# Kernel optimization log

Measured on AMD Instinct MI355X. Metric: run time of the kernel, lower is better.

Reference implementation:

```python
import jax, jax.numpy as jnp
import numpy as np

H_DIM = 1024
HEAD_DIM = 128
N_HEADS = 8
HD = HEAD_DIM * N_HEADS  # 1024


def setup_inputs() -> dict:
    key = jax.random.key(0)
    ks = jax.random.split(key, 32)
    B, S = 16, 1024
    inp = {
        "f_in": jax.random.normal(ks[0], (B, S, H_DIM), jnp.float32),
        "i_in": jax.random.normal(ks[1], (B, S, H_DIM), jnp.float32),
        "z_in": jax.random.normal(ks[2], (B, S, H_DIM), jnp.float32),
        "o_in": jax.random.normal(ks[3], (B, S, H_DIM), jnp.float32),
        "c0": jax.random.normal(ks[4], (B, N_HEADS, HEAD_DIM), jnp.float32),
        "h0": jax.random.normal(ks[5], (B, N_HEADS, HEAD_DIM), jnp.float32),
    }
    # Parameters (torch Linear stored here as [in, out]; init std=0.02, zero bias)
    names_x = ["Fx", "Ix", "Zx", "Ox"]
    names_h = ["Fh", "Ih", "Zh", "Oh"]
    for j, n in enumerate(names_x):
        inp[f"W_{n}"] = 0.02 * jax.random.normal(ks[6 + j], (H_DIM, HD), jnp.float32)
        inp[f"b_{n}"] = jnp.zeros((HD,), jnp.float32)
    for j, n in enumerate(names_h):
        inp[f"W_{n}"] = 0.02 * jax.random.normal(ks[10 + j], (HD, HD), jnp.float32)
        inp[f"b_{n}"] = jnp.zeros((HD,), jnp.float32)
    inp["W_post"] = 0.02 * jax.random.normal(ks[14], (HD, H_DIM), jnp.float32)
    inp["b_post"] = jnp.zeros((H_DIM,), jnp.float32)
    return inp


def reference(f_in, i_in, z_in, o_in, c0, h0,
              W_Fx, b_Fx, W_Ix, b_Ix, W_Zx, b_Zx, W_Ox, b_Ox,
              W_Fh, b_Fh, W_Ih, b_Ih, W_Zh, b_Zh, W_Oh, b_Oh,
              W_post, b_post):
    B, S, _ = f_in.shape
    # Precompute input-to-gate projections for all timesteps: (B,S,HD)
    fx = f_in @ W_Fx + b_Fx
    ix = i_in @ W_Ix + b_Ix
    zx = z_in @ W_Zx + b_Zx
    ox = o_in @ W_Ox + b_Ox
    # Flatten head state: gating is elementwise, heads are contiguous in HD
    c = c0.reshape(B, HD)
    h = h0.reshape(B, HD)
    # Time-major for scan: (S,B,HD)
    xs = (fx.transpose(1, 0, 2), ix.transpose(1, 0, 2),
          zx.transpose(1, 0, 2), ox.transpose(1, 0, 2))

    def step(carry, x):
        c, h = carry
        fx_t, ix_t, zx_t, ox_t = x
        f = jax.nn.sigmoid(fx_t + h @ W_Fh + b_Fh)
        i = jax.nn.sigmoid(ix_t + h @ W_Ih + b_Ih)
        z = jnp.tanh(zx_t + h @ W_Zh + b_Zh)
        o = jax.nn.sigmoid(ox_t + h @ W_Oh + b_Oh)
        c = f * c + i * z
        h = o * jnp.tanh(c)
        return (c, h), h

    (c, h), ys = jax.lax.scan(step, (c, h), xs)
    y = ys.transpose(1, 0, 2)  # (B,S,HD)
    y = y @ W_post + b_post    # n_heads > 1 -> post-head projection
    state = (c.reshape(B, N_HEADS, HEAD_DIM), h.reshape(B, N_HEADS, HEAD_DIM))
    return (y, state)
```

## Files before the change

### kernel.cpp

```cpp
#include <hip/hip_runtime.h>
#include <stdint.h>
#include <stddef.h>

typedef __attribute__((ext_vector_type(8))) short short8;
typedef __attribute__((ext_vector_type(4))) short short4_t;
typedef __attribute__((ext_vector_type(8))) unsigned short ushort8_t;
typedef __attribute__((ext_vector_type(4))) unsigned short ushort4_t;
typedef __attribute__((ext_vector_type(4))) float f32x4;
typedef __attribute__((ext_vector_type(4))) unsigned uint4_t;

#define XG_BYTES  (134217728ull)
#define HS_BYTES  (33587200ull)
#define PAD_OFF   (XG_BYTES + HS_BYTES)
#define WT_OFF    (PAD_OFF + 32768ull)

#define SENT 0x7FC07FC0u

__device__ __forceinline__ unsigned short f2b(float f){
  unsigned u = __builtin_bit_cast(unsigned, f);
  u += 0x7fffu + ((u >> 16) & 1u);
  return (unsigned short)(u >> 16);
}
__device__ __forceinline__ float b2f(unsigned short b){
  unsigned u = ((unsigned)b) << 16;
  return __builtin_bit_cast(float, u);
}
__device__ __forceinline__ float sigm(float x){ return 1.0f / (1.0f + __expf(-x)); }
__device__ __forceinline__ float tanh_(float x){ return 2.0f / (1.0f + __expf(-2.0f*x)) - 1.0f; }

__device__ __forceinline__ void ld_h8_plain(const unsigned short* p, short8* a){
  asm volatile(
    "global_load_dwordx4 %0, %8, off\n\t"
    "global_load_dwordx4 %1, %8, off offset:64\n\t"
    "global_load_dwordx4 %2, %8, off offset:128\n\t"
    "global_load_dwordx4 %3, %8, off offset:192\n\t"
    "global_load_dwordx4 %4, %8, off offset:256\n\t"
    "global_load_dwordx4 %5, %8, off offset:320\n\t"
    "global_load_dwordx4 %6, %8, off offset:384\n\t"
    "global_load_dwordx4 %7, %8, off offset:448\n\t"
    "s_waitcnt vmcnt(0)"
    : "=&v"(a[0]), "=&v"(a[1]), "=&v"(a[2]), "=&v"(a[3]),
      "=&v"(a[4]), "=&v"(a[5]), "=&v"(a[6]), "=&v"(a[7])
    : "v"(p) : "memory");
}
__device__ __forceinline__ void st_u32_mall(unsigned* p, unsigned v){
  asm volatile("global_store_dword %0, %1, off sc0 sc1"
               :: "v"(p), "v"(v) : "memory");
}

__global__ __launch_bounds__(256) void k_prep(
    const float* __restrict__ w0, const float* __restrict__ w1,
    const float* __restrict__ w2, const float* __restrict__ w3,
    const float* __restrict__ w4, const float* __restrict__ w5,
    const float* __restrict__ w6, const float* __restrict__ w7,
    const float* __restrict__ w8, unsigned short* __restrict__ wt)
{
  const int z = blockIdx.z;
  const float* W = (z==0)?w0:(z==1)?w1:(z==2)?w2:(z==3)?w3:(z==4)?w4:
                   (z==5)?w5:(z==6)?w6:(z==7)?w7:w8;
  unsigned short* out = wt + (size_t)z*1024*1024;
  __shared__ float tile[64][65];
  const int k0 = blockIdx.x*64, n0 = blockIdx.y*64;
  const int tid = threadIdx.x;
  {
    const int kk = tid >> 2, nn0 = (tid & 3) * 16;
    const float* src = W + (size_t)(k0+kk)*1024 + n0 + nn0;
    #pragma unroll
    for (int j=0;j<16;j+=4){
      f32x4 v = *(const f32x4*)(src + j);
      tile[kk][nn0+j+0]=v[0]; tile[kk][nn0+j+1]=v[1];
      tile[kk][nn0+j+2]=v[2]; tile[kk][nn0+j+3]=v[3];
    }
  }
  __syncthreads();
  {
    const int nn = tid >> 2, kk0 = (tid & 3) * 16;
    ushort8_t a, b;
    #pragma unroll
    for (int j=0;j<8;++j){ a[j]=f2b(tile[kk0+j][nn]); b[j]=f2b(tile[kk0+8+j][nn]); }
    unsigned short* dst = out + (size_t)(n0+nn)*1024 + k0 + kk0;
    *(ushort8_t*)dst = a;
    *(ushort8_t*)(dst+8) = b;
  }
}

__global__ void k_init(const float* __restrict__ h0, unsigned short* __restrict__ hs){
  const int i = blockIdx.x*256 + threadIdx.x;
  unsigned v = (unsigned)f2b(h0[i]);
  asm volatile("global_store_short %0, %1, off sc0 sc1"
               :: "v"(hs + i), "v"(v) : "memory");
}

__global__ void k_fill(unsigned* __restrict__ hsw){
  const size_t i = (size_t)blockIdx.x*256 + threadIdx.x;
  uint4_t v = (uint4_t){SENT, SENT, SENT, SENT};
  asm volatile("global_store_dwordx4 %0, %1, off sc0 sc1"
               :: "v"(hsw + 8192 + i*4), "v"(v) : "memory");
}

__global__ __launch_bounds__(256,2) void k_xproj(
    const float* __restrict__ xF, const float* __restrict__ xI,
    const float* __restrict__ xZ, const float* __restrict__ xO,
    const float* __restrict__ bF, const float* __restrict__ bI,
    const float* __restrict__ bZ, const float* __restrict__ bO,
    const unsigned short* __restrict__ Wt,
    unsigned short* __restrict__ xg)
{
  const int g  = blockIdx.z;
  const int tm = blockIdx.x, tn = blockIdx.y;
  const float* X  = (g==0)?xF:(g==1)?xI:(g==2)?xZ:xO;
  const float* Bp = (g==0)?bF:(g==1)?bI:(g==2)?bZ:bO;
  const unsigned short* Wg = Wt + (size_t)g*1024*1024;

  __shared__ unsigned short Asm[128*32];
  __shared__ unsigned short Bsm[128*32];

  const int tid  = threadIdx.x;
  const int lane = tid & 63, wv = tid >> 6;
  const int l15  = lane & 15, lg = lane >> 4;
  const int wy   = wv >> 1,  wx = wv & 1;

  const int rr = tid >> 1, kq = tid & 1;
  const int ar = tm*128 + rr;
  const int ab = ar & 15, as_ = ar >> 4;
  const float* aptr = X + ((size_t)ab*1024 + as_)*1024 + kq*16;
  const unsigned short* bp_ = Wg + (size_t)(tn*128 + rr)*1024 + kq*16;
  const int s0 = kq*2;
  unsigned short* aw0 = &Asm[rr*32 + (((s0  ) ^ (rr&3))<<3)];
  unsigned short* aw1 = &Asm[rr*32 + (((s0+1) ^ (rr&3))<<3)];
  unsigned short* bw0 = &Bsm[rr*32 + (((s0  ) ^ (rr&3))<<3)];
  unsigned short* bw1 = &Bsm[rr*32 + (((s0+1) ^ (rr&3))<<3)];

  f32x4 acc[4][4];
  #pragma unroll
  for (int m=0;m<4;++m)
    #pragma unroll
    for (int q=0;q<4;++q) acc[m][q] = (f32x4){0.f,0.f,0.f,0.f};

  for (int k0=0; k0<1024; k0+=32){
    const float* ap = aptr + k0;
    f32x4 v0 = *(const f32x4*)(ap + 0);
    f32x4 v1 = *(const f32x4*)(ap + 4);
    f32x4 v2 = *(const f32x4*)(ap + 8);
    f32x4 v3 = *(const f32x4*)(ap + 12);
    ushort8_t pa, pb;
    #pragma unroll
    for (int j=0;j<4;++j){ pa[j]=f2b(v0[j]); pa[4+j]=f2b(v1[j]); pb[j]=f2b(v2[j]); pb[4+j]=f2b(v3[j]); }
    *(ushort8_t*)aw0 = pa;
    *(ushort8_t*)aw1 = pb;
    ushort8_t q0 = *(const ushort8_t*)(bp_ + k0);
    ushort8_t q1 = *(const ushort8_t*)(bp_ + k0 + 8);
    *(ushort8_t*)bw0 = q0;
    *(ushort8_t*)bw1 = q1;
    __syncthreads();

    short8 af[4], bf_[4];
    #pragma unroll
    for (int m=0;m<4;++m){
      int row = wy*64 + m*16 + l15;
      af[m] = *(const short8*)&Asm[row*32 + ((lg ^ (row&3))<<3)];
    }
    #pragma unroll
    for (int q=0;q<4;++q){
      int row = wx*64 + q*16 + l15;
      bf_[q] = *(const short8*)&Bsm[row*32 + ((lg ^ (row&3))<<3)];
    }
    #pragma unroll
    for (int m=0;m<4;++m)
      #pragma unroll
      for (int q=0;q<4;++q)
        acc[m][q] = __builtin_amdgcn_mfma_f32_16x16x32_bf16(af[m], bf_[q], acc[m][q], 0,0,0);
    __syncthreads();
  }

  #pragma unroll
  for (int m=0;m<4;++m){
    const int t = tm*8 + wy*4 + m;
    #pragma unroll
    for (int q=0;q<4;++q){
      const int n = tn*128 + wx*64 + q*16 + l15;
      const float bias = Bp[n];
      f32x4 v = acc[m][q];
      ushort4_t pk;
      #pragma unroll
      for (int r=0;r<4;++r) pk[r] = f2b(v[r] + bias);
      *(ushort4_t*)(xg + (size_t)((t*4+g)*1024 + n)*16 + lg*4) = pk;
    }
  }
}

__global__ __launch_bounds__(256,1) void k_recur(
    const unsigned short* __restrict__ WtR,
    const float* __restrict__ bfh, const float* __restrict__ bih,
    const float* __restrict__ bzh, const float* __restrict__ boh,
    const float* __restrict__ c0,
    const unsigned short* __restrict__ xg,
    unsigned short* __restrict__ hs,
    float* __restrict__ oc, float* __restrict__ oh)
{
  const int wg   = blockIdx.x;
  const int tid  = threadIdx.x;
  const int wv   = tid >> 6, lane = tid & 63;
  const int l15  = lane & 15, lg = lane >> 4;
  const int n    = wg*16 + l15;

  short8 wf[4][8];
  #pragma unroll
  for (int g=0; g<4; ++g){
    const unsigned short* wp = WtR + (size_t)g*1048576 + (size_t)n*1024 + wv*256 + lg*8;
    #pragma unroll
    for (int c=0; c<8; ++c)
      wf[g][c] = *(const short8*)(wp + c*32);
  }

  float cst[4]; float bias[4];
  bias[0]=bfh[n]; bias[1]=bih[n]; bias[2]=bzh[n]; bias[3]=boh[n];
  #pragma unroll
  for (int r=0;r<4;++r) cst[r] = c0[(size_t)(lg*4+r)*1024 + n];

  __shared__ f32x4 part[2][4][4][64];

  unsigned* hsw = (unsigned*)hs;
  const int koff = l15*1024 + wv*256 + lg*8;

  float hv = 0.f;
  for (int t=0; t<1024; ++t){
    short4_t xq[4];
    #pragma unroll
    for (int g=0; g<4; ++g)
      xq[g] = *(const short4_t*)(xg + (size_t)((t*4+g)*1024 + n)*16 + lg*4);

    const unsigned short* hp = hs + (size_t)t*16384 + koff;
    short8 a[8];
    ld_h8_plain(hp, a);
    {
      bool bad[8]; bool any = false;
      #pragma unroll
      for (int c=0;c<8;++c){
        uint4_t q = __builtin_bit_cast(uint4_t, a[c]);
        bad[c] = (q[0]==SENT)||(q[1]==SENT)||(q[2]==SENT)||(q[3]==SENT);
        any = any | bad[c];
      }
      while (__any(any)){
        __builtin_amdgcn_s_sleep(1);
        #pragma unroll
        for (int c=0;c<8;++c)
          if (bad[c])
            asm volatile("global_load_dwordx4 %0, %1, off sc0 sc1"
                         : "+v"(a[c]) : "v"(hp + c*32) : "memory");
        asm volatile("s_waitcnt vmcnt(0)" ::: "memory");
        __builtin_amdgcn_sched_barrier(0);
        any = false;
        #pragma unroll
        for (int c=0;c<8;++c){
          uint4_t q = __builtin_bit_cast(uint4_t, a[c]);
          bad[c] = (q[0]==SENT)||(q[1]==SENT)||(q[2]==SENT)||(q[3]==SENT);
          any = any | bad[c];
        }
      }
    }

    f32x4 acc[4];
    #pragma unroll
    for (int g=0;g<4;++g) acc[g] = (f32x4){0.f,0.f,0.f,0.f};
    #pragma unroll
    for (int c=0;c<8;++c){
      acc[0] = __builtin_amdgcn_mfma_f32_16x16x32_bf16(a[c], wf[0][c], acc[0], 0,0,0);
      acc[1] = __builtin_amdgcn_mfma_f32_16x16x32_bf16(a[c], wf[1][c], acc[1], 0,0,0);
      acc[2] = __builtin_amdgcn_mfma_f32_16x16x32_bf16(a[c], wf[2][c], acc[2], 0,0,0);
      acc[3] = __builtin_amdgcn_mfma_f32_16x16x32_bf16(a[c], wf[3][c], acc[3], 0,0,0);
    }
    const int pb = t & 1;
    #pragma unroll
    for (int g=0;g<4;++g) part[pb][wv][g][lane] = acc[g];
    __syncthreads();

    f32x4 r_[4];
    #pragma unroll
    for (int g=0;g<4;++g){
      f32x4 s0 = part[pb][0][g][lane];
      f32x4 s1 = part[pb][1][g][lane];
      f32x4 s2 = part[pb][2][g][lane];
      f32x4 s3 = part[pb][3][g][lane];
      r_[g] = (s0 + s1) + (s2 + s3);
    }

    float hvv[4];
    {
      const int r = wv;
      float pf = r_[0][r] + b2f((unsigned short)xq[0][r]) + bias[0];
      float pi = r_[1][r] + b2f((unsigned short)xq[1][r]) + bias[1];
      float pz = r_[2][r] + b2f((unsigned short)xq[2][r]) + bias[2];
      float po = r_[3][r] + b2f((unsigned short)xq[3][r]) + bias[3];
      float fg = sigm(pf), ig = sigm(pi), zg = tanh_(pz), og = sigm(po);
      float cn = fg*cst[r] + ig*zg;
      cst[r] = cn;
      hv = og * tanh_(cn);
      hvv[r] = hv;
      unsigned m  = (unsigned)f2b(hv);
      unsigned nb = (unsigned)__shfl_xor(m, 1);
      if ((l15 & 1) == 0){
        unsigned word = m | (nb << 16);
        unsigned* pw = hsw + (size_t)(t+1)*8192 + (size_t)(lg*4+wv)*512 + (n >> 1);
        st_u32_mall(pw, word);
      }
    }
    #pragma unroll
    for (int r=0;r<4;++r){
      if (r == wv) continue;
      float pf = r_[0][r] + b2f((unsigned short)xq[0][r]) + bias[0];
      float pi = r_[1][r] + b2f((unsigned short)xq[1][r]) + bias[1];
      float pz = r_[2][r] + b2f((unsigned short)xq[2][r]) + bias[2];
      float po = r_[3][r] + b2f((unsigned short)xq[3][r]) + bias[3];
      float fg = sigm(pf), ig = sigm(pi), zg = tanh_(pz), og = sigm(po);
      float cn = fg*cst[r] + ig*zg;
      cst[r] = cn;
      hvv[r] = og * tanh_(cn);
    }
    if (t == 1023 && wv == 0){
      #pragma unroll
      for (int r=0;r<4;++r){
        oc[(size_t)(lg*4+r)*1024 + n] = cst[r];
        oh[(size_t)(lg*4+r)*1024 + n] = hvv[r];
      }
    }
  }
}

__global__ __launch_bounds__(256,2) void k_post(
    const unsigned short* __restrict__ hs,
    const unsigned short* __restrict__ Wt,
    const float* __restrict__ bpost,
    float* __restrict__ y)
{
  const int tm = blockIdx.x, tn = blockIdx.y;
  __shared__ unsigned short Asm[128*32];
  __shared__ unsigned short Bsm[128*32];

  const int tid  = threadIdx.x;
  const int lane = tid & 63, wv = tid >> 6;
  const int l15  = lane & 15, lg = lane >> 4;
  const int wy   = wv >> 1,  wx = wv & 1;

  const int rr = tid >> 1, kq = tid & 1;
  const unsigned short* aptr = hs + 16384 + (size_t)(tm*128 + rr)*1024 + kq*16;
  const unsigned short* bp_  = Wt + (size_t)4*1024*1024 + (size_t)(tn*128 + rr)*1024 + kq*16;
  const int s0 = kq*2;
  unsigned short* aw0 = &Asm[rr*32 + (((s0  ) ^ (rr&3))<<3)];
  unsigned short* aw1 = &Asm[rr*32 + (((s0+1) ^ (rr&3))<<3)];
  unsigned short* bw0 = &Bsm[rr*32 + (((s0  ) ^ (rr&3))<<3)];
  unsigned short* bw1 = &Bsm[rr*32 + (((s0+1) ^ (rr&3))<<3)];

  f32x4 acc[4][4];
  #pragma unroll
  for (int m=0;m<4;++m)
    #pragma unroll
    for (int q=0;q<4;++q) acc[m][q] = (f32x4){0.f,0.f,0.f,0.f};

  for (int k0=0; k0<1024; k0+=32){
    ushort8_t a0 = *(const ushort8_t*)(aptr + k0);
    ushort8_t a1 = *(const ushort8_t*)(aptr + k0 + 8);
    *(ushort8_t*)aw0 = a0;
    *(ushort8_t*)aw1 = a1;
    ushort8_t q0 = *(const ushort8_t*)(bp_ + k0);
    ushort8_t q1 = *(const ushort8_t*)(bp_ + k0 + 8);
    *(ushort8_t*)bw0 = q0;
    *(ushort8_t*)bw1 = q1;
    __syncthreads();

    short8 af[4], bf_[4];
    #pragma unroll
    for (int m=0;m<4;++m){
      int row = wy*64 + m*16 + l15;
      af[m] = *(const short8*)&Asm[row*32 + ((lg ^ (row&3))<<3)];
    }
    #pragma unroll
    for (int q=0;q<4;++q){
      int row = wx*64 + q*16 + l15;
      bf_[q] = *(const short8*)&Bsm[row*32 + ((lg ^ (row&3))<<3)];
    }
    #pragma unroll
    for (int m=0;m<4;++m)
      #pragma unroll
      for (int q=0;q<4;++q)
        acc[m][q] = __builtin_amdgcn_mfma_f32_16x16x32_bf16(af[m], bf_[q], acc[m][q], 0,0,0);
    __syncthreads();
  }

  #pragma unroll
  for (int m=0;m<4;++m){
    const int s = tm*8 + wy*4 + m;
    #pragma unroll
    for (int q=0;q<4;++q){
      const int n = tn*128 + wx*64 + q*16 + l15;
      const float bias = bpost[n];
      f32x4 v = acc[m][q];
      #pragma unroll
      for (int r=0;r<4;++r){
        const int b = lg*4 + r;
        y[((size_t)b << 20) + ((size_t)s << 10) + n] = v[r] + bias;
      }
    }
  }
}

extern "C" void kernel_launch(void* const* d_in, const int* in_sizes, int n_in,
                              void* d_out, int out_size, void* d_ws, size_t ws_size,
                              hipStream_t stream)
{
  const float* f_in = (const float*)d_in[0];
  const float* i_in = (const float*)d_in[1];
  const float* z_in = (const float*)d_in[2];
  const float* o_in = (const float*)d_in[3];
  const float* c0   = (const float*)d_in[4];
  const float* h0   = (const float*)d_in[5];
  const float* W_Fx = (const float*)d_in[6];  const float* b_Fx = (const float*)d_in[7];
  const float* W_Ix = (const float*)d_in[8];  const float* b_Ix = (const float*)d_in[9];
  const float* W_Zx = (const float*)d_in[10]; const float* b_Zx = (const float*)d_in[11];
  const float* W_Ox = (const float*)d_in[12]; const float* b_Ox = (const float*)d_in[13];
  const float* W_Fh = (const float*)d_in[14]; const float* b_Fh = (const float*)d_in[15];
  const float* W_Ih = (const float*)d_in[16]; const float* b_Ih = (const float*)d_in[17];
  const float* W_Zh = (const float*)d_in[18]; const float* b_Zh = (const float*)d_in[19];
  const float* W_Oh = (const float*)d_in[20]; const float* b_Oh = (const float*)d_in[21];
  const float* W_post = (const float*)d_in[22]; const float* b_post = (const float*)d_in[23];

  char* ws = (char*)d_ws;
  unsigned short* xg    = (unsigned short*)(ws);
  unsigned short* hs    = (unsigned short*)(ws + XG_BYTES);
  unsigned short* wt    = (unsigned short*)(ws + WT_OFF);

  float* y  = (float*)d_out;
  float* oc = y + 16777216;
  float* oh = oc + 16384;

  k_prep<<<dim3(16,16,9), 256, 0, stream>>>(W_Fx, W_Ix, W_Zx, W_Ox, W_post,
                                            W_Fh, W_Ih, W_Zh, W_Oh, wt);
  k_init<<<64, 256, 0, stream>>>(h0, hs);
  k_fill<<<8192, 256, 0, stream>>>((unsigned*)hs);
  k_xproj<<<dim3(128,8,4), 256, 0, stream>>>(f_in, i_in, z_in, o_in,
                                             b_Fx, b_Ix, b_Zx, b_Ox, wt, xg);
  k_recur<<<64, 256, 0, stream>>>(wt + (size_t)5*1024*1024,
                                  b_Fh, b_Ih, b_Zh, b_Oh,
                                  c0, xg, hs, oc, oh);
  k_post<<<dim3(128,8), 256, 0, stream>>>(hs, wt, b_post, y);
}
```

Measured before the change: 3.728 ms.

## Fuse xproj, recurrence and post projection into one persistent overlapped kernel

Merges the input projection, the recurrent scan and the post-head projection into a single kernel. Its first 64 blocks run the recurrence while the remaining 192 blocks compute the input GEMMs and then the post GEMM. Workspace is pre-filled with sentinel values so consumers spin on them, letting the projection and post stages overlap with the serial scan instead of running before and after it. The costs are a larger sentinel fill of the xg buffer, polling overhead, and a reliance on all 256 blocks being co-resident to avoid deadlock.

```diff
diff --git a/kernel.cpp b/kernel.cpp
--- a/kernel.cpp
+++ b/kernel.cpp
@@ -8,6 +8,7 @@
 typedef __attribute__((ext_vector_type(4))) unsigned short ushort4_t;
 typedef __attribute__((ext_vector_type(4))) float f32x4;
 typedef __attribute__((ext_vector_type(4))) unsigned uint4_t;
+typedef __attribute__((ext_vector_type(2))) unsigned uint2_t;
 
 #define XG_BYTES  (134217728ull)
 #define HS_BYTES  (33587200ull)
@@ -91,314 +92,365 @@
                :: "v"(hs + i), "v"(v) : "memory");
 }
 
-__global__ void k_fill(unsigned* __restrict__ hsw){
+__global__ void k_fill(unsigned* __restrict__ xgw, unsigned* __restrict__ hsw){
   const size_t i = (size_t)blockIdx.x*256 + threadIdx.x;
   uint4_t v = (uint4_t){SENT, SENT, SENT, SENT};
-  asm volatile("global_store_dwordx4 %0, %1, off sc0 sc1"
-               :: "v"(hsw + 8192 + i*4), "v"(v) : "memory");
-}
-
-__global__ __launch_bounds__(256,2) void k_xproj(
+  if (i < 8388608ull){
+    asm volatile("global_store_dwordx4 %0, %1, off sc0 sc1"
+                 :: "v"(xgw + i*4), "v"(v) : "memory");
+  } else {
+    asm volatile("global_store_dwordx4 %0, %1, off sc0 sc1"
+                 :: "v"(hsw + 8192 + (i - 8388608ull)*4), "v"(v) : "memory");
+  }
+}
+
+__global__ __launch_bounds__(256,1) void k_mega(
     const float* __restrict__ xF, const float* __restrict__ xI,
     const float* __restrict__ xZ, const float* __restrict__ xO,
     const float* __restrict__ bF, const float* __restrict__ bI,
     const float* __restrict__ bZ, const float* __restrict__ bO,
-    const unsigned short* __restrict__ Wt,
-    unsigned short* __restrict__ xg)
+    const unsigned short* __restrict__ wt,
+    const float* __restrict__ bfh, const float* __restrict__ bih,
+    const float* __restrict__ bzh, const float* __restrict__ boh,
+    const float* __restrict__ c0,
+    unsigned short* __restrict__ xg,
+    unsigned short* __restrict__ hs,
+    const float* __restrict__ bpost,
+    float* __restrict__ y,
+    float* __restrict__ oc, float* __restrict__ oh)
 {
-  const int g  = blockIdx.z;
-  const int tm = blockIdx.x, tn = blockIdx.y;
-  const float* X  = (g==0)?xF:(g==1)?xI:(g==2)?xZ:xO;
-  const float* Bp = (g==0)?bF:(g==1)?bI:(g==2)?bZ:bO;
-  const unsigned short* Wg = Wt + (size_t)g*1024*1024;
-
-  __shared__ unsigned short Asm[128*32];
-  __shared__ unsigned short Bsm[128*32];
-
+  __shared__ __align__(16) char smem[32768];
   const int tid  = threadIdx.x;
   const int lane = tid & 63, wv = tid >> 6;
   const int l15  = lane & 15, lg = lane >> 4;
-  const int wy   = wv >> 1,  wx = wv & 1;
-
-  const int rr = tid >> 1, kq = tid & 1;
-  const int ar = tm*128 + rr;
-  const int ab = ar & 15, as_ = ar >> 4;
-  const float* aptr = X + ((size_t)ab*1024 + as_)*1024 + kq*16;
-  const unsigned short* bp_ = Wg + (size_t)(tn*128 + rr)*1024 + kq*16;
-  const int s0 = kq*2;
-  unsigned short* aw0 = &Asm[rr*32 + (((s0  ) ^ (rr&3))<<3)];
-  unsigned short* aw1 = &Asm[rr*32 + (((s0+1) ^ (rr&3))<<3)];
-  unsigned short* bw0 = &Bsm[rr*32 + (((s0  ) ^ (rr&3))<<3)];
-  unsigned short* bw1 = &Bsm[rr*32 + (((s0+1) ^ (rr&3))<<3)];
-
-  f32x4 acc[4][4];
-  #pragma unroll
-  for (int m=0;m<4;++m)
-    #pragma unroll
-    for (int q=0;q<4;++q) acc[m][q] = (f32x4){0.f,0.f,0.f,0.f};
-
-  for (int k0=0; k0<1024; k0+=32){
-    const float* ap = aptr + k0;
-    f32x4 v0 = *(const f32x4*)(ap + 0);
-    f32x4 v1 = *(const f32x4*)(ap + 4);
-    f32x4 v2 = *(const f32x4*)(ap + 8);
-    f32x4 v3 = *(const f32x4*)(ap + 12);
-    ushort8_t pa, pb;
-    #pragma unroll
-    for (int j=0;j<4;++j){ pa[j]=f2b(v0[j]); pa[4+j]=f2b(v1[j]); pb[j]=f2b(v2[j]); pb[4+j]=f2b(v3[j]); }
-    *(ushort8_t*)aw0 = pa;
-    *(ushort8_t*)aw1 = pb;
-    ushort8_t q0 = *(const ushort8_t*)(bp_ + k0);
-    ushort8_t q1 = *(const ushort8_t*)(bp_ + k0 + 8);
-    *(ushort8_t*)bw0 = q0;
-    *(ushort8_t*)bw1 = q1;
-    __syncthreads();
-
-    short8 af[4], bf_[4];
-    #pragma unroll
-    for (int m=0;m<4;++m){
-      int row = wy*64 + m*16 + l15;
-      af[m] = *(const short8*)&Asm[row*32 + ((lg ^ (row&3))<<3)];
-    }
-    #pragma unroll
-    for (int q=0;q<4;++q){
-      int row = wx*64 + q*16 + l15;
-      bf_[q] = *(const short8*)&Bsm[row*32 + ((lg ^ (row&3))<<3)];
-    }
-    #pragma unroll
-    for (int m=0;m<4;++m)
-      #pragma unroll
-      for (int q=0;q<4;++q)
-        acc[m][q] = __builtin_amdgcn_mfma_f32_16x16x32_bf16(af[m], bf_[q], acc[m][q], 0,0,0);
-    __syncthreads();
-  }
-
-  #pragma unroll
-  for (int m=0;m<4;++m){
-    const int t = tm*8 + wy*4 + m;
-    #pragma unroll
-    for (int q=0;q<4;++q){
-      const int n = tn*128 + wx*64 + q*16 + l15;
-      const float bias = Bp[n];
-      f32x4 v = acc[m][q];
-      ushort4_t pk;
-      #pragma unroll
-      for (int r=0;r<4;++r) pk[r] = f2b(v[r] + bias);
-      *(ushort4_t*)(xg + (size_t)((t*4+g)*1024 + n)*16 + lg*4) = pk;
-    }
-  }
-}
-
-__global__ __launch_bounds__(256,1) void k_recur(
-    const unsigned short* __restrict__ WtR,
-    const float* __restrict__ bfh, const float* __restrict__ bih,
-    const float* __restrict__ bzh, const float* __restrict__ boh,
-    const float* __restrict__ c0,
-    const unsigned short* __restrict__ xg,
-    unsigned short* __restrict__ hs,
-    float* __restrict__ oc, float* __restrict__ oh)
-{
-  const int wg   = blockIdx.x;
-  const int tid  = threadIdx.x;
-  const int wv   = tid >> 6, lane = tid & 63;
-  const int l15  = lane & 15, lg = lane >> 4;
-  const int n    = wg*16 + l15;
-
-  short8 wf[4][8];
-  #pragma unroll
-  for (int g=0; g<4; ++g){
-    const unsigned short* wp = WtR + (size_t)g*1048576 + (size_t)n*1024 + wv*256 + lg*8;
-    #pragma unroll
-    for (int c=0; c<8; ++c)
-      wf[g][c] = *(const short8*)(wp + c*32);
-  }
-
-  float cst[4]; float bias[4];
-  bias[0]=bfh[n]; bias[1]=bih[n]; bias[2]=bzh[n]; bias[3]=boh[n];
-  #pragma unroll
-  for (int r=0;r<4;++r) cst[r] = c0[(size_t)(lg*4+r)*1024 + n];
-
-  __shared__ f32x4 part[2][4][4][64];
-
-  unsigned* hsw = (unsigned*)hs;
-  const int koff = l15*1024 + wv*256 + lg*8;
-
-  float hv = 0.f;
-  for (int t=0; t<1024; ++t){
-    short4_t xq[4];
-    #pragma unroll
-    for (int g=0; g<4; ++g)
-      xq[g] = *(const short4_t*)(xg + (size_t)((t*4+g)*1024 + n)*16 + lg*4);
-
-    const unsigned short* hp = hs + (size_t)t*16384 + koff;
-    short8 a[8];
-    ld_h8_plain(hp, a);
-    {
-      bool bad[8]; bool any = false;
-      #pragma unroll
-      for (int c=0;c<8;++c){
-        uint4_t q = __builtin_bit_cast(uint4_t, a[c]);
-        bad[c] = (q[0]==SENT)||(q[1]==SENT)||(q[2]==SENT)||(q[3]==SENT);
-        any = any | bad[c];
-      }
-      while (__any(any)){
-        __builtin_amdgcn_s_sleep(1);
-        #pragma unroll
-        for (int c=0;c<8;++c)
-          if (bad[c])
-            asm volatile("global_load_dwordx4 %0, %1, off sc0 sc1"
-                         : "+v"(a[c]) : "v"(hp + c*32) : "memory");
-        asm volatile("s_waitcnt vmcnt(0)" ::: "memory");
-        __builtin_amdgcn_sched_barrier(0);
-        any = false;
+
+  if (blockIdx.x < 64){
+    typedef f32x4 PartT[4][4][64];
+    PartT* part = (PartT*)smem;
+
+    const unsigned short* WtR = wt + (size_t)5*1048576;
+    const int wg = blockIdx.x;
+    const int n  = wg*16 + l15;
+
+    short8 wf[4][8];
+    #pragma unroll
+    for (int g=0; g<4; ++g){
+      const unsigned short* wp = WtR + (size_t)g*1048576 + (size_t)n*1024 + wv*256 + lg*8;
+      #pragma unroll
+      for (int c=0; c<8; ++c)
+        wf[g][c] = *(const short8*)(wp + c*32);
+    }
+
+    float cst[4]; float bias[4];
+    bias[0]=bfh[n]; bias[1]=bih[n]; bias[2]=bzh[n]; bias[3]=boh[n];
+    #pragma unroll
+    for (int r=0;r<4;++r) cst[r] = c0[(size_t)(lg*4+r)*1024 + n];
+
+    unsigned* hsw = (unsigned*)hs;
+    const int koff = l15*1024 + wv*256 + lg*8;
+
+    float hv = 0.f;
+    for (int t=0; t<1024; ++t){
+      short4_t xq[4];
+      {
+        const unsigned short* xb = xg + (size_t)((t*4)*1024 + n)*16 + lg*4;
+        asm volatile(
+          "global_load_dwordx2 %0, %4, off\n\t"
+          "global_load_dwordx2 %1, %5, off\n\t"
+          "global_load_dwordx2 %2, %6, off\n\t"
+          "global_load_dwordx2 %3, %7, off"
+          : "=&v"(xq[0]), "=&v"(xq[1]), "=&v"(xq[2]), "=&v"(xq[3])
+          : "v"(xb), "v"(xb + 16384), "v"(xb + 32768), "v"(xb + 49152)
+          : "memory");
+      }
+
+      const unsigned short* hp = hs + (size_t)t*16384 + koff;
+      short8 a[8];
+      ld_h8_plain(hp, a);
+      {
+        bool bad[8]; bool any = false;
         #pragma unroll
         for (int c=0;c<8;++c){
           uint4_t q = __builtin_bit_cast(uint4_t, a[c]);
           bad[c] = (q[0]==SENT)||(q[1]==SENT)||(q[2]==SENT)||(q[3]==SENT);
           any = any | bad[c];
         }
-      }
-    }
-
-    f32x4 acc[4];
-    #pragma unroll
-    for (int g=0;g<4;++g) acc[g] = (f32x4){0.f,0.f,0.f,0.f};
-    #pragma unroll
-    for (int c=0;c<8;++c){
-      acc[0] = __builtin_amdgcn_mfma_f32_16x16x32_bf16(a[c], wf[0][c], acc[0], 0,0,0);
-      acc[1] = __builtin_amdgcn_mfma_f32_16x16x32_bf16(a[c], wf[1][c], acc[1], 0,0,0);
-      acc[2] = __builtin_amdgcn_mfma_f32_16x16x32_bf16(a[c], wf[2][c], acc[2], 0,0,0);
-      acc[3] = __builtin_amdgcn_mfma_f32_16x16x32_bf16(a[c], wf[3][c], acc[3], 0,0,0);
-    }
-    const int pb = t & 1;
-    #pragma unroll
-    for (int g=0;g<4;++g) part[pb][wv][g][lane] = acc[g];
-    __syncthreads();
-
-    f32x4 r_[4];
-    #pragma unroll
-    for (int g=0;g<4;++g){
-      f32x4 s0 = part[pb][0][g][lane];
-      f32x4 s1 = part[pb][1][g][lane];
-      f32x4 s2 = part[pb][2][g][lane];
-      f32x4 s3 = part[pb][3][g][lane];
-      r_[g] = (s0 + s1) + (s2 + s3);
-    }
-
-    float hvv[4];
-    {
-      const int r = wv;
-      float pf = r_[0][r] + b2f((unsigned short)xq[0][r]) + bias[0];
-      float pi = r_[1][r] + b2f((unsigned short)xq[1][r]) + bias[1];
-      float pz = r_[2][r] + b2f((unsigned short)xq[2][r]) + bias[2];
-      float po = r_[3][r] + b2f((unsigned short)xq[3][r]) + bias[3];
-      float fg = sigm(pf), ig = sigm(pi), zg = tanh_(pz), og = sigm(po);
-      float cn = fg*cst[r] + ig*zg;
-      cst[r] = cn;
-      hv = og * tanh_(cn);
-      hvv[r] = hv;
-      unsigned m  = (unsigned)f2b(hv);
-      unsigned nb = (unsigned)__shfl_xor(m, 1);
-      if ((l15 & 1) == 0){
-        unsigned word = m | (nb << 16);
-        unsigned* pw = hsw + (size_t)(t+1)*8192 + (size_t)(lg*4+wv)*512 + (n >> 1);
-        st_u32_mall(pw, word);
-      }
-    }
-    #pragma unroll
-    for (int r=0;r<4;++r){
-      if (r == wv) continue;
-      float pf = r_[0][r] + b2f((unsigned short)xq[0][r]) + bias[0];
-      float pi = r_[1][r] + b2f((unsigned short)xq[1][r]) + bias[1];
-      float pz = r_[2][r] + b2f((unsigned short)xq[2][r]) + bias[2];
-      float po = r_[3][r] + b2f((unsigned short)xq[3][r]) + bias[3];
-      float fg = sigm(pf), ig = sigm(pi), zg = tanh_(pz), og = sigm(po);
-      float cn = fg*cst[r] + ig*zg;
-      cst[r] = cn;
-      hvv[r] = og * tanh_(cn);
-    }
-    if (t == 1023 && wv == 0){
+        while (__any(any)){
+          __builtin_amdgcn_s_sleep(1);
+          #pragma unroll
+          for (int c=0;c<8;++c)
+            if (bad[c])
+              asm volatile("global_load_dwordx4 %0, %1, off sc0 sc1"
+                           : "+v"(a[c]) : "v"(hp + c*32) : "memory");
+          asm volatile("s_waitcnt vmcnt(0)" ::: "memory");
+          __builtin_amdgcn_sched_barrier(0);
+          any = false;
+          #pragma unroll
+          for (int c=0;c<8;++c){
+            uint4_t q = __builtin_bit_cast(uint4_t, a[c]);
+            bad[c] = (q[0]==SENT)||(q[1]==SENT)||(q[2]==SENT)||(q[3]==SENT);
+            any = any | bad[c];
+          }
+        }
+      }
+      {
+        bool xb_[4]; bool anyx = false;
+        #pragma unroll
+        for (int g=0; g<4; ++g){
+          uint2_t u = __builtin_bit_cast(uint2_t, xq[g]);
+          xb_[g] = (u[0]==SENT)||(u[1]==SENT);
+          anyx = anyx | xb_[g];
+        }
+        while (__any(anyx)){
+          __builtin_amdgcn_s_sleep(2);
+          const unsigned short* xb = xg + (size_t)((t*4)*1024 + n)*16 + lg*4;
+          #pragma unroll
+          for (int g=0; g<4; ++g)
+            if (xb_[g])
+              asm volatile("global_load_dwordx2 %0, %1, off sc0 sc1"
+                           : "+v"(xq[g]) : "v"(xb + g*16384) : "memory");
+          asm volatile("s_waitcnt vmcnt(0)" ::: "memory");
+          __builtin_amdgcn_sched_barrier(0);
+          anyx = false;
+          #pragma unroll
+          for (int g=0; g<4; ++g){
+            uint2_t u = __builtin_bit_cast(uint2_t, xq[g]);
+            xb_[g] = (u[0]==SENT)||(u[1]==SENT);
+            anyx = anyx | xb_[g];
+          }
+        }
+      }
+
+      f32x4 acc[4];
+      #pragma unroll
+      for (int g=0;g<4;++g) acc[g] = (f32x4){0.f,0.f,0.f,0.f};
+      #pragma unroll
+      for (int c=0;c<8;++c){
+        acc[0] = __builtin_amdgcn_mfma_f32_16x16x32_bf16(a[c], wf[0][c], acc[0], 0,0,0);
+        acc[1] = __builtin_amdgcn_mfma_f32_16x16x32_bf16(a[c], wf[1][c], acc[1], 0,0,0);
+        acc[2] = __builtin_amdgcn_mfma_f32_16x16x32_bf16(a[c], wf[2][c], acc[2], 0,0,0);
+        acc[3] = __builtin_amdgcn_mfma_f32_16x16x32_bf16(a[c], wf[3][c], acc[3], 0,0,0);
+      }
+      const int pb = t & 1;
+      #pragma unroll
+      for (int g=0;g<4;++g) part[pb][wv][g][lane] = acc[g];
+      __syncthreads();
+
+      f32x4 r_[4];
+      #pragma unroll
+      for (int g=0;g<4;++g){
+        f32x4 s0 = part[pb][0][g][lane];
+        f32x4 s1 = part[pb][1][g][lane];
+        f32x4 s2 = part[pb][2][g][lane];
+        f32x4 s3 = part[pb][3][g][lane];
+        r_[g] = (s0 + s1) + (s2 + s3);
+      }
+
+      float hvv[4];
+      {
+        const int r = wv;
+        float pf = r_[0][r] + b2f((unsigned short)xq[0][r]) + bias[0];
+        float pi = r_[1][r] + b2f((unsigned short)xq[1][r]) + bias[1];
+        float pz = r_[2][r] + b2f((unsigned short)xq[2][r]) + bias[2];
+        float po = r_[3][r] + b2f((unsigned short)xq[3][r]) + bias[3];
+        float fg = sigm(pf), ig = sigm(pi), zg = tanh_(pz), og = sigm(po);
+        float cn = fg*cst[r] + ig*zg;
+        cst[r] = cn;
+        hv = og * tanh_(cn);
+        hvv[r] = hv;
+        unsigned m  = (unsigned)f2b(hv);
+        unsigned nb = (unsigned)__shfl_xor(m, 1);
+        if ((l15 & 1) == 0){
+          unsigned word = m | (nb << 16);
+          unsigned* pw = hsw + (size_t)(t+1)*8192 + (size_t)(lg*4+wv)*512 + (n >> 1);
+          st_u32_mall(pw, word);
+        }
+      }
       #pragma unroll
       for (int r=0;r<4;++r){
-        oc[(size_t)(lg*4+r)*1024 + n] = cst[r];
-        oh[(size_t)(lg*4+r)*1024 + n] = hvv[r];
-      }
-    }
-  }
-}
-
-__global__ __launch_bounds__(256,2) void k_post(
-    const unsigned short* __restrict__ hs,
-    const unsigned short* __restrict__ Wt,
-    const float* __restrict__ bpost,
-    float* __restrict__ y)
-{
-  const int tm = blockIdx.x, tn = blockIdx.y;
-  __shared__ unsigned short Asm[128*32];
-  __shared__ unsigned short Bsm[128*32];
-
-  const int tid  = threadIdx.x;
-  const int lane = tid & 63, wv = tid >> 6;
-  const int l15  = lane & 15, lg = lane >> 4;
-  const int wy   = wv >> 1,  wx = wv & 1;
-
+        if (r == wv) continue;
+        float pf = r_[0][r] + b2f((unsigned short)xq[0][r]) + bias[0];
+        float pi = r_[1][r] + b2f((unsigned short)xq[1][r]) + bias[1];
+        float pz = r_[2][r] + b2f((unsigned short)xq[2][r]) + bias[2];
+        float po = r_[3][r] + b2f((unsigned short)xq[3][r]) + bias[3];
+        float fg = sigm(pf), ig = sigm(pi), zg = tanh_(pz), og = sigm(po);
+        float cn = fg*cst[r] + ig*zg;
+        cst[r] = cn;
+        hvv[r] = og * tanh_(cn);
+      }
+      if (t == 1023 && wv == 0){
+        #pragma unroll
+        for (int r=0;r<4;++r){
+          oc[(size_t)(lg*4+r)*1024 + n] = cst[r];
+          oh[(size_t)(lg*4+r)*1024 + n] = hvv[r];
+        }
+      }
+    }
+    return;
+  }
+
+  unsigned short* AsmB = (unsigned short*)smem;
+  unsigned short* BsmB = (unsigned short*)(smem + 8192);
+  const int wid = blockIdx.x - 64;
+  const int wy = wv >> 1, wx = wv & 1;
   const int rr = tid >> 1, kq = tid & 1;
-  const unsigned short* aptr = hs + 16384 + (size_t)(tm*128 + rr)*1024 + kq*16;
-  const unsigned short* bp_  = Wt + (size_t)4*1024*1024 + (size_t)(tn*128 + rr)*1024 + kq*16;
   const int s0 = kq*2;
-  unsigned short* aw0 = &Asm[rr*32 + (((s0  ) ^ (rr&3))<<3)];
-  unsigned short* aw1 = &Asm[rr*32 + (((s0+1) ^ (rr&3))<<3)];
-  unsigned short* bw0 = &Bsm[rr*32 + (((s0  ) ^ (rr&3))<<3)];
-  unsigned short* bw1 = &Bsm[rr*32 + (((s0+1) ^ (rr&3))<<3)];
-
-  f32x4 acc[4][4];
-  #pragma unroll
-  for (int m=0;m<4;++m)
-    #pragma unroll
-    for (int q=0;q<4;++q) acc[m][q] = (f32x4){0.f,0.f,0.f,0.f};
-
-  for (int k0=0; k0<1024; k0+=32){
-    ushort8_t a0 = *(const ushort8_t*)(aptr + k0);
-    ushort8_t a1 = *(const ushort8_t*)(aptr + k0 + 8);
-    *(ushort8_t*)aw0 = a0;
-    *(ushort8_t*)aw1 = a1;
-    ushort8_t q0 = *(const ushort8_t*)(bp_ + k0);
-    ushort8_t q1 = *(const ushort8_t*)(bp_ + k0 + 8);
-    *(ushort8_t*)bw0 = q0;
-    *(ushort8_t*)bw1 = q1;
-    __syncthreads();
-
-    short8 af[4], bf_[4];
+  unsigned short* aw0 = &AsmB[rr*32 + (((s0  ) ^ (rr&3))<<3)];
+  unsigned short* aw1 = &AsmB[rr*32 + (((s0+1) ^ (rr&3))<<3)];
+  unsigned short* bw0 = &BsmB[rr*32 + (((s0  ) ^ (rr&3))<<3)];
+  unsigned short* bw1 = &BsmB[rr*32 + (((s0+1) ^ (rr&3))<<3)];
+
+  for (int idx = wid; idx < 4096; idx += 192){
+    const int tm = idx >> 5, rmn = idx & 31, tn = rmn >> 2, g = rmn & 3;
+    const float* X  = (g==0)?xF:(g==1)?xI:(g==2)?xZ:xO;
+    const float* Bp = (g==0)?bF:(g==1)?bI:(g==2)?bZ:bO;
+    const unsigned short* Wg = wt + (size_t)g*1048576;
+
+    const int ar = tm*128 + rr;
+    const int ab = ar & 15, as_ = ar >> 4;
+    const float* aptr = X + ((size_t)ab*1024 + as_)*1024 + kq*16;
+    const unsigned short* bp_ = Wg + (size_t)(tn*128 + rr)*1024 + kq*16;
+
+    f32x4 acc[4][4];
+    #pragma unroll
+    for (int m=0;m<4;++m)
+      #pragma unroll
+      for (int q=0;q<4;++q) acc[m][q] = (f32x4){0.f,0.f,0.f,0.f};
+
+    for (int k0=0; k0<1024; k0+=32){
+      const float* ap = aptr + k0;
+      f32x4 v0 = *(const f32x4*)(ap + 0);
+      f32x4 v1 = *(const f32x4*)(ap + 4);
+      f32x4 v2 = *(const f32x4*)(ap + 8);
+      f32x4 v3 = *(const f32x4*)(ap + 12);
+      ushort8_t pa, pb;
+      #pragma unroll
+      for (int j=0;j<4;++j){ pa[j]=f2b(v0[j]); pa[4+j]=f2b(v1[j]); pb[j]=f2b(v2[j]); pb[4+j]=f2b(v3[j]); }
+      *(ushort8_t*)aw0 = pa;
+      *(ushort8_t*)aw1 = pb;
+      ushort8_t q0 = *(const ushort8_t*)(bp_ + k0);
+      ushort8_t q1 = *(const ushort8_t*)(bp_ + k0 + 8);
+      *(ushort8_t*)bw0 = q0;
+      *(ushort8_t*)bw1 = q1;
+      __syncthreads();
+
+      short8 af[4], bf_[4];
+      #pragma unroll
+      for (int m=0;m<4;++m){
+        int row = wy*64 + m*16 + l15;
+        af[m] = *(const short8*)&AsmB[row*32 + ((lg ^ (row&3))<<3)];
+      }
+      #pragma unroll
+      for (int q=0;q<4;++q){
+        int row = wx*64 + q*16 + l15;
+        bf_[q] = *(const short8*)&BsmB[row*32 + ((lg ^ (row&3))<<3)];
+      }
+      #pragma unroll
+      for (int m=0;m<4;++m)
+        #pragma unroll
+        for (int q=0;q<4;++q)
+          acc[m][q] = __builtin_amdgcn_mfma_f32_16x16x32_bf16(af[m], bf_[q], acc[m][q], 0,0,0);
+      __syncthreads();
+    }
+
     #pragma unroll
     for (int m=0;m<4;++m){
-      int row = wy*64 + m*16 + l15;
-      af[m] = *(const short8*)&Asm[row*32 + ((lg ^ (row&3))<<3)];
-    }
-    #pragma unroll
-    for (int q=0;q<4;++q){
-      int row = wx*64 + q*16 + l15;
-      bf_[q] = *(const short8*)&Bsm[row*32 + ((lg ^ (row&3))<<3)];
-    }
+      const int t = tm*8 + wy*4 + m;
+      #pragma unroll
+      for (int q=0;q<4;++q){
+        const int n = tn*128 + wx*64 + q*16 + l15;
+        const float bias = Bp[n];
+        f32x4 v = acc[m][q];
+        ushort4_t pk;
+        #pragma unroll
+        for (int r=0;r<4;++r) pk[r] = f2b(v[r] + bias);
+        uint2_t w2 = __builtin_bit_cast(uint2_t, pk);
+        unsigned short* dst = xg + (size_t)((t*4+g)*1024 + n)*16 + lg*4;
+        asm volatile("global_store_dwordx2 %0, %1, off sc0 sc1"
+                     :: "v"(dst), "v"(w2) : "memory");
+      }
+    }
+  }
+
+  for (int idx = wid; idx < 1024; idx += 192){
+    const int tm = idx >> 3, tn = idx & 7;
+    const unsigned short* aptr = hs + 16384 + (size_t)(tm*128 + rr)*1024 + kq*16;
+    const unsigned short* bp_  = wt + (size_t)4*1048576 + (size_t)(tn*128 + rr)*1024 + kq*16;
+
+    f32x4 acc[4][4];
     #pragma unroll
     for (int m=0;m<4;++m)
       #pragma unroll
-      for (int q=0;q<4;++q)
-        acc[m][q] = __builtin_amdgcn_mfma_f32_16x16x32_bf16(af[m], bf_[q], acc[m][q], 0,0,0);
-    __syncthreads();
-  }
-
-  #pragma unroll
-  for (int m=0;m<4;++m){
-    const int s = tm*8 + wy*4 + m;
-    #pragma unroll
-    for (int q=0;q<4;++q){
-      const int n = tn*128 + wx*64 + q*16 + l15;
-      const float bias = bpost[n];
-      f32x4 v = acc[m][q];
-      #pragma unroll
-      for (int r=0;r<4;++r){
-        const int b = lg*4 + r;
-        y[((size_t)b << 20) + ((size_t)s << 10) + n] = v[r] + bias;
+      for (int q=0;q<4;++q) acc[m][q] = (f32x4){0.f,0.f,0.f,0.f};
+
+    for (int k0=0; k0<1024; k0+=32){
+      ushort8_t a0, a1;
+      asm volatile(
+        "global_load_dwordx4 %0, %2, off\n\t"
+        "global_load_dwordx4 %1, %3, off\n\t"
+        "s_waitcnt vmcnt(0)"
+        : "=&v"(a0), "=&v"(a1)
+        : "v"(aptr + k0), "v"(aptr + k0 + 8) : "memory");
+      __builtin_amdgcn_sched_barrier(0);
+      {
+        uint4_t q0 = __builtin_bit_cast(uint4_t, a0);
+        uint4_t q1 = __builtin_bit_cast(uint4_t, a1);
+        bool b0 = (q0[0]==SENT)||(q0[1]==SENT)||(q0[2]==SENT)||(q0[3]==SENT);
+        bool b1 = (q1[0]==SENT)||(q1[1]==SENT)||(q1[2]==SENT)||(q1[3]==SENT);
+        while (__any(b0 | b1)){
+          __builtin_amdgcn_s_sleep(8);
+          if (b0) asm volatile("global_load_dwordx4 %0, %1, off sc0 sc1"
+                               : "+v"(a0) : "v"(aptr + k0) : "memory");
+          if (b1) asm volatile("global_load_dwordx4 %0, %1, off sc0 sc1"
+                               : "+v"(a1) : "v"(aptr + k0 + 8) : "memory");
+          asm volatile("s_waitcnt vmcnt(0)" ::: "memory");
+          __builtin_amdgcn_sched_barrier(0);
+          q0 = __builtin_bit_cast(uint4_t, a0);
+          q1 = __builtin_bit_cast(uint4_t, a1);
+          b0 = (q0[0]==SENT)||(q0[1]==SENT)||(q0[2]==SENT)||(q0[3]==SENT);
+          b1 = (q1[0]==SENT)||(q1[1]==SENT)||(q1[2]==SENT)||(q1[3]==SENT);
+        }
+      }
+      *(ushort8_t*)aw0 = a0;
+      *(ushort8_t*)aw1 = a1;
+      ushort8_t q0v = *(const ushort8_t*)(bp_ + k0);
+      ushort8_t q1v = *(const ushort8_t*)(bp_ + k0 + 8);
+      *(ushort8_t*)bw0 = q0v;
+      *(ushort8_t*)bw1 = q1v;
+      __syncthreads();
+
+      short8 af[4], bf_[4];
+      #pragma unroll
+      for (int m=0;m<4;++m){
+        int row = wy*64 + m*16 + l15;
+        af[m] = *(const short8*)&AsmB[row*32 + ((lg ^ (row&3))<<3)];
+      }
+      #pragma unroll
+      for (int q=0;q<4;++q){
+        int row = wx*64 + q*16 + l15;
+        bf_[q] = *(const short8*)&BsmB[row*32 + ((lg ^ (row&3))<<3)];
+      }
+      #pragma unroll
+      for (int m=0;m<4;++m)
+        #pragma unroll
+        for (int q=0;q<4;++q)
+          acc[m][q] = __builtin_amdgcn_mfma_f32_16x16x32_bf16(af[m], bf_[q], acc[m][q], 0,0,0);
+      __syncthreads();
+    }
+
+    #pragma unroll
+    for (int m=0;m<4;++m){
+      const int s = tm*8 + wy*4 + m;
+      #pragma unroll
+      for (int q=0;q<4;++q){
+        const int n = tn*128 + wx*64 + q*16 + l15;
+        const float bias = bpost[n];
+        f32x4 v = acc[m][q];
+        #pragma unroll
+        for (int r=0;r<4;++r){
+          const int b = lg*4 + r;
+          y[((size_t)b << 20) + ((size_t)s << 10) + n] = v[r] + bias;
+        }
       }
     }
   }
@@ -425,9 +477,9 @@
   const float* W_post = (const float*)d_in[22]; const float* b_post = (const float*)d_in[23];
 
   char* ws = (char*)d_ws;
-  unsigned short* xg    = (unsigned short*)(ws);
-  unsigned short* hs    = (unsigned short*)(ws + XG_BYTES);
-  unsigned short* wt    = (unsigned short*)(ws + WT_OFF);
+  unsigned short* xg = (unsigned short*)(ws);
+  unsigned short* hs = (unsigned short*)(ws + XG_BYTES);
+  unsigned short* wt = (unsigned short*)(ws + WT_OFF);
 
   float* y  = (float*)d_out;
   float* oc = y + 16777216;
@@ -436,11 +488,10 @@
   k_prep<<<dim3(16,16,9), 256, 0, stream>>>(W_Fx, W_Ix, W_Zx, W_Ox, W_post,
                                             W_Fh, W_Ih, W_Zh, W_Oh, wt);
   k_init<<<64, 256, 0, stream>>>(h0, hs);
-  k_fill<<<8192, 256, 0, stream>>>((unsigned*)hs);
-  k_xproj<<<dim3(128,8,4), 256, 0, stream>>>(f_in, i_in, z_in, o_in,
-                                             b_Fx, b_Ix, b_Zx, b_Ox, wt, xg);
-  k_recur<<<64, 256, 0, stream>>>(wt + (size_t)5*1024*1024,
+  k_fill<<<40960, 256, 0, stream>>>((unsigned*)xg, (unsigned*)hs);
+  k_mega<<<256, 256, 0, stream>>>(f_in, i_in, z_in, o_in,
+                                  b_Fx, b_Ix, b_Zx, b_Ox,
+                                  wt,
                                   b_Fh, b_Ih, b_Zh, b_Oh,
-                                  c0, xg, hs, oc, oh);
-  k_post<<<dim3(128,8), 256, 0, stream>>>(hs, wt, b_post, y);
-}
+                                  c0, xg, hs, b_post, y, oc, oh);
+}
```

Measured after the change: 3.556 ms. 4.6% less time.
